# Performance work log

Measured on AMD Instinct MI355X. Metric: run time of the kernel, lower is better.

## Reference

```python
import jax, jax.numpy as jnp
import numpy as np


def build_weights(target):
    """Vectorized version of the per-(batch,frame) distance-weight loop.

    target: [B, T, W, W]. For each frame, find the mean (row, col) coordinate
    of the maximal pixels, then weight = W / (dist_to_center + 1).
    """
    W = target.shape[-1]
    m = jnp.max(target, axis=(-2, -1), keepdims=True)
    mask = (target == m).astype(target.dtype)          # [B,T,W,W]
    cnt = jnp.sum(mask, axis=(-2, -1))                 # [B,T]
    idx = jnp.arange(W, dtype=target.dtype)            # [W]
    # mean row index x and mean col index y of argmax pixels
    x = jnp.sum(jnp.sum(mask, axis=-1) * idx, axis=-1) / cnt  # [B,T]
    y = jnp.sum(jnp.sum(mask, axis=-2) * idx, axis=-1) / cnt  # [B,T]
    a = idx[None, None, :, None] - x[:, :, None, None]  # row offsets [B,T,W,1]
    b = idx[None, None, None, :] - y[:, :, None, None]  # col offsets [B,T,1,W]
    dist = jnp.sqrt(a * a + b * b)                      # [B,T,W,W]
    return W / (dist + 1.0)  # reciprocal of (sqrt(dist)+1)/W


def setup_inputs() -> dict:
    key = jax.random.key(0)
    k1, k2 = jax.random.split(key)
    B, T, W = 16, 16, 256
    inp = jax.random.uniform(k1, (B, 1, T, W, W), dtype=jnp.float32)
    tgt = jax.random.uniform(k2, (B, T, W, W), dtype=jnp.float32)
    return {"input": inp, "target": tgt}


def reference(input, target):
    p = jnp.squeeze(input, axis=1)                 # [B,T,W,W]
    w = build_weights(target)
    # torch binary_cross_entropy clamps log terms at -100
    logp = jnp.clip(jnp.log(p), -100.0)
    log1mp = jnp.clip(jnp.log1p(-p), -100.0)
    loss = -jnp.mean(w * (target * logp + (1.0 - target) * log1mp))
    return loss
```

## Files before the change

kernel.cpp:

```cpp
#include <hip/hip_runtime.h>

#define WDIM 256
#define FRAME (WDIM * WDIM)
#define NFRAMES 256
#define NTOT ((long long)NFRAMES * FRAME)

#define ACC_OFFSET 16384

__device__ inline void monoid_merge(float& m, float& cnt, float& sr, float& sc,
                                    float m2, float cnt2, float sr2, float sc2) {
    if (m2 > m) { m = m2; cnt = cnt2; sr = sr2; sc = sc2; }
    else if (m2 == m) { cnt += cnt2; sr += sr2; sc += sc2; }
}

__global__ __launch_bounds__(256)
void floss_partial(const float* __restrict__ target, float4* __restrict__ partials,
                   double* __restrict__ acc) {
    const int blk = blockIdx.x;
    const int frame = blk >> 2;
    const int quarter = blk & 3;
    const int tid = threadIdx.x;
    const int lane = tid & 63, wave = tid >> 6;

    if (blk == 0 && tid == 0) *acc = 0.0;

    const float4* __restrict__ t4 =
        (const float4*)(target + (size_t)frame * FRAME) + quarter * 4096 + tid;

    float4 v[16];
    #pragma unroll
    for (int k = 0; k < 16; ++k) v[k] = t4[k * 256];

    const float rowb = (float)(quarter * 64 + wave);
    const float colb = (float)(lane * 4);

    float m = -1.0f, cnt = 0.0f, sr = 0.0f, sc = 0.0f;
    #pragma unroll
    for (int k = 0; k < 16; ++k) {
        const float row = rowb + (float)(4 * k);
        const float vv[4] = {v[k].x, v[k].y, v[k].z, v[k].w};
        #pragma unroll
        for (int j = 0; j < 4; ++j) {
            const float val = vv[j];
            const float col = colb + (float)j;
            if (val > m)       { m = val; cnt = 1.0f; sr = row; sc = col; }
            else if (val == m) { cnt += 1.0f; sr += row; sc += col; }
        }
    }
    #pragma unroll
    for (int off = 32; off > 0; off >>= 1) {
        float m2  = __shfl_down(m, off);
        float c2  = __shfl_down(cnt, off);
        float sr2 = __shfl_down(sr, off);
        float sc2 = __shfl_down(sc, off);
        monoid_merge(m, cnt, sr, sc, m2, c2, sr2, sc2);
    }
    __shared__ float sm[4], scnt[4], ssr[4], ssc[4];
    if (lane == 0) { sm[wave] = m; scnt[wave] = cnt; ssr[wave] = sr; ssc[wave] = sc; }
    __syncthreads();
    if (tid == 0) {
        m = sm[0]; cnt = scnt[0]; sr = ssr[0]; sc = ssc[0];
        #pragma unroll
        for (int w2 = 1; w2 < 4; ++w2)
            monoid_merge(m, cnt, sr, sc, sm[w2], scnt[w2], ssr[w2], ssc[w2]);
        partials[blk] = make_float4(m, cnt, sr, sc);
    }
}

__global__ __launch_bounds__(256)
void floss_bce(const float* __restrict__ input, const float* __restrict__ target,
               const float4* __restrict__ partials, double* __restrict__ acc) {
    const int blk = blockIdx.x;
    const int frame = blk >> 3;
    const int seg = blk & 7;
    const int tid = threadIdx.x;
    const int lane = tid & 63, wave = tid >> 6;

    const float4* __restrict__ t4 =
        (const float4*)(target + (size_t)frame * FRAME) + seg * 2048 + tid;
    const float4* __restrict__ p4 =
        (const float4*)(input + (size_t)frame * FRAME) + seg * 2048 + tid;

    float4 tv[8], pv[8];
    #pragma unroll
    for (int k = 0; k < 8; ++k) { tv[k] = t4[k * 256]; pv[k] = p4[k * 256]; }

    float m, cnt, sr, sc;
    {
        const float4 p0 = partials[frame * 4 + 0];
        m = p0.x; cnt = p0.y; sr = p0.z; sc = p0.w;
        #pragma unroll
        for (int q = 1; q < 4; ++q) {
            const float4 pq = partials[frame * 4 + q];
            monoid_merge(m, cnt, sr, sc, pq.x, pq.y, pq.z, pq.w);
        }
    }
    const float rc = __builtin_amdgcn_rcpf(cnt);
    const float x = sr * rc;
    const float y = sc * rc;

    const float drb = (float)(seg * 32 + wave) - x;
    const float dcb = (float)(lane * 4) - y;
    float dc2[4];
    #pragma unroll
    for (int j = 0; j < 4; ++j) { const float d = dcb + (float)j; dc2[j] = d * d; }

    float acc0 = 0.0f, acc1 = 0.0f;
    #pragma unroll
    for (int k = 0; k < 8; ++k) {
        const float dr = drb + (float)(4 * k);
        const float dr2 = dr * dr;
        const float tvv[4] = {tv[k].x, tv[k].y, tv[k].z, tv[k].w};
        const float pvv[4] = {pv[k].x, pv[k].y, pv[k].z, pv[k].w};
        #pragma unroll
        for (int j = 0; j < 4; ++j) {
            const float dist = __builtin_amdgcn_sqrtf(dr2 + dc2[j]);
            const float w = 256.0f * __builtin_amdgcn_rcpf(dist + 1.0f);
            const float tt = tvv[j], pp = pvv[j];
            const float lp  = fmaxf(__logf(pp), -100.0f);
            const float l1p = fmaxf(__logf(1.0f - pp), -100.0f);
            if (j & 1) acc1 += w * fmaf(tt, lp - l1p, l1p);
            else       acc0 += w * fmaf(tt, lp - l1p, l1p);
        }
    }
    float local = acc0 + acc1;
    #pragma unroll
    for (int off = 32; off > 0; off >>= 1) local += __shfl_down(local, off);
    __shared__ float sacc[4];
    if (lane == 0) sacc[wave] = local;
    __syncthreads();
    if (tid == 0) {
        atomicAdd(acc, (double)(sacc[0] + sacc[1] + sacc[2] + sacc[3]));
    }
}

__global__ void floss_final(const double* __restrict__ acc, float* __restrict__ out) {
    if (threadIdx.x == 0 && blockIdx.x == 0)
        out[0] = (float)(-acc[0] / (double)NTOT);
}

extern "C" void kernel_launch(void* const* d_in, const int* in_sizes, int n_in,
                              void* d_out, int out_size, void* d_ws, size_t ws_size,
                              hipStream_t stream) {
    const float* input  = (const float*)d_in[0];
    const float* target = (const float*)d_in[1];
    float* out = (float*)d_out;
    float4* partials = (float4*)d_ws;
    double* acc = (double*)((char*)d_ws + ACC_OFFSET);

    floss_partial<<<NFRAMES * 4, 256, 0, stream>>>(target, partials, acc);
    floss_bce<<<NFRAMES * 8, 256, 0, stream>>>(input, target, partials, acc);
    floss_final<<<1, 64, 0, stream>>>(acc, out);
}
```

Measured before the change: 159.4 us.

## Fuse argmax and BCE passes per frame, caching target as bf16 in LDS

```diff
diff --git a/kernel.cpp b/kernel.cpp
--- a/kernel.cpp
+++ b/kernel.cpp
@@ -1,11 +1,13 @@
 #include <hip/hip_runtime.h>
+#include <hip/hip_bf16.h>
+#include <string.h>
 
 #define WDIM 256
 #define FRAME (WDIM * WDIM)
 #define NFRAMES 256
 #define NTOT ((long long)NFRAMES * FRAME)
+#define BLOCK 1024
 
-#define ACC_OFFSET 16384
 
 __device__ inline void monoid_merge(float& m, float& cnt, float& sr, float& sc,
                                     float m2, float cnt2, float sr2, float sc2) {
@@ -13,39 +15,41 @@
     else if (m2 == m) { cnt += cnt2; sr += sr2; sc += sc2; }
 }
 
-__global__ __launch_bounds__(256)
-void floss_partial(const float* __restrict__ target, float4* __restrict__ partials,
-                   double* __restrict__ acc) {
-    const int blk = blockIdx.x;
-    const int frame = blk >> 2;
-    const int quarter = blk & 3;
+__device__ inline unsigned int pack_bf16x2(float a, float b) {
+    __hip_bfloat162 h = __float22bfloat162_rn(make_float2(a, b));
+    unsigned int u; memcpy(&u, &h, 4); return u;
+}
+
+__global__ __launch_bounds__(BLOCK, 4)
+void floss_fused(const float* __restrict__ input, const float* __restrict__ target,
+                 double* __restrict__ blocksum) {
+    __shared__ unsigned int lds_t[FRAME / 2];
+    __shared__ float sm[16], scnt[16], ssr[16], ssc[16];
+    __shared__ float sx, sy;
+
+    const int frame = blockIdx.x;
     const int tid = threadIdx.x;
     const int lane = tid & 63, wave = tid >> 6;
 
-    if (blk == 0 && tid == 0) *acc = 0.0;
+    const float4* __restrict__ t4 = (const float4*)(target + (size_t)frame * FRAME);
+    const float4* __restrict__ p4 = (const float4*)(input  + (size_t)frame * FRAME);
 
-    const float4* __restrict__ t4 =
-        (const float4*)(target + (size_t)frame * FRAME) + quarter * 4096 + tid;
-
-    float4 v[16];
-    #pragma unroll
-    for (int k = 0; k < 16; ++k) v[k] = t4[k * 256];
-
-    const float rowb = (float)(quarter * 64 + wave);
     const float colb = (float)(lane * 4);
-
     float m = -1.0f, cnt = 0.0f, sr = 0.0f, sc = 0.0f;
     #pragma unroll
     for (int k = 0; k < 16; ++k) {
-        const float row = rowb + (float)(4 * k);
-        const float vv[4] = {v[k].x, v[k].y, v[k].z, v[k].w};
+        const int i4 = k * 1024 + tid;
+        const float4 v = t4[i4];
+        const float row = (float)(16 * k + wave);
+        const float vv[4] = {v.x, v.y, v.z, v.w};
         #pragma unroll
         for (int j = 0; j < 4; ++j) {
             const float val = vv[j];
-            const float col = colb + (float)j;
-            if (val > m)       { m = val; cnt = 1.0f; sr = row; sc = col; }
-            else if (val == m) { cnt += 1.0f; sr += row; sc += col; }
+            if (val > m)       { m = val; cnt = 1.0f; sr = row; sc = colb + (float)j; }
+            else if (val == m) { cnt += 1.0f; sr += row; sc += colb + (float)j; }
         }
+        *(uint2*)&lds_t[2 * i4] =
+            make_uint2(pack_bf16x2(v.x, v.y), pack_bf16x2(v.z, v.w));
     }
     #pragma unroll
     for (int off = 32; off > 0; off >>= 1) {
@@ -55,88 +59,79 @@
         float sc2 = __shfl_down(sc, off);
         monoid_merge(m, cnt, sr, sc, m2, c2, sr2, sc2);
     }
-    __shared__ float sm[4], scnt[4], ssr[4], ssc[4];
     if (lane == 0) { sm[wave] = m; scnt[wave] = cnt; ssr[wave] = sr; ssc[wave] = sc; }
     __syncthreads();
     if (tid == 0) {
         m = sm[0]; cnt = scnt[0]; sr = ssr[0]; sc = ssc[0];
         #pragma unroll
-        for (int w2 = 1; w2 < 4; ++w2)
+        for (int w2 = 1; w2 < 16; ++w2)
             monoid_merge(m, cnt, sr, sc, sm[w2], scnt[w2], ssr[w2], ssc[w2]);
-        partials[blk] = make_float4(m, cnt, sr, sc);
+        const float rc = __builtin_amdgcn_rcpf(cnt);
+        sx = sr * rc;
+        sy = sc * rc;
     }
-}
+    __syncthreads();
+    const float x = sx, y = sy;
 
-__global__ __launch_bounds__(256)
-void floss_bce(const float* __restrict__ input, const float* __restrict__ target,
-               const float4* __restrict__ partials, double* __restrict__ acc) {
-    const int blk = blockIdx.x;
-    const int frame = blk >> 3;
-    const int seg = blk & 7;
-    const int tid = threadIdx.x;
-    const int lane = tid & 63, wave = tid >> 6;
-
-    const float4* __restrict__ t4 =
-        (const float4*)(target + (size_t)frame * FRAME) + seg * 2048 + tid;
-    const float4* __restrict__ p4 =
-        (const float4*)(input + (size_t)frame * FRAME) + seg * 2048 + tid;
-
-    float4 tv[8], pv[8];
-    #pragma unroll
-    for (int k = 0; k < 8; ++k) { tv[k] = t4[k * 256]; pv[k] = p4[k * 256]; }
-
-    float m, cnt, sr, sc;
-    {
-        const float4 p0 = partials[frame * 4 + 0];
-        m = p0.x; cnt = p0.y; sr = p0.z; sc = p0.w;
-        #pragma unroll
-        for (int q = 1; q < 4; ++q) {
-            const float4 pq = partials[frame * 4 + q];
-            monoid_merge(m, cnt, sr, sc, pq.x, pq.y, pq.z, pq.w);
-        }
-    }
-    const float rc = __builtin_amdgcn_rcpf(cnt);
-    const float x = sr * rc;
-    const float y = sc * rc;
-
-    const float drb = (float)(seg * 32 + wave) - x;
-    const float dcb = (float)(lane * 4) - y;
+    const float drb = (float)wave - x;
     float dc2[4];
     #pragma unroll
-    for (int j = 0; j < 4; ++j) { const float d = dcb + (float)j; dc2[j] = d * d; }
+    for (int j = 0; j < 4; ++j) {
+        const float d = colb + (float)j - y;
+        dc2[j] = d * d;
+    }
 
     float acc0 = 0.0f, acc1 = 0.0f;
     #pragma unroll
-    for (int k = 0; k < 8; ++k) {
-        const float dr = drb + (float)(4 * k);
+    for (int k = 0; k < 16; ++k) {
+        const int i4 = k * 1024 + tid;
+        const float4 pvv = p4[i4];
+        const uint2 tw = *(const uint2*)&lds_t[2 * i4];
+        const float tvv[4] = {
+            __uint_as_float(tw.x << 16),
+            __uint_as_float(tw.x & 0xffff0000u),
+            __uint_as_float(tw.y << 16),
+            __uint_as_float(tw.y & 0xffff0000u)
+        };
+        const float pp[4] = {pvv.x, pvv.y, pvv.z, pvv.w};
+        const float dr = drb + (float)(16 * k);
         const float dr2 = dr * dr;
-        const float tvv[4] = {tv[k].x, tv[k].y, tv[k].z, tv[k].w};
-        const float pvv[4] = {pv[k].x, pv[k].y, pv[k].z, pv[k].w};
         #pragma unroll
         for (int j = 0; j < 4; ++j) {
             const float dist = __builtin_amdgcn_sqrtf(dr2 + dc2[j]);
             const float w = 256.0f * __builtin_amdgcn_rcpf(dist + 1.0f);
-            const float tt = tvv[j], pp = pvv[j];
-            const float lp  = fmaxf(__logf(pp), -100.0f);
-            const float l1p = fmaxf(__logf(1.0f - pp), -100.0f);
-            if (j & 1) acc1 += w * fmaf(tt, lp - l1p, l1p);
-            else       acc0 += w * fmaf(tt, lp - l1p, l1p);
+            const float p = pp[j];
+            const float lp  = fmaxf(__logf(p), -100.0f);
+            const float l1p = fmaxf(__logf(1.0f - p), -100.0f);
+            if (j & 1) acc1 += w * fmaf(tvv[j], lp - l1p, l1p);
+            else       acc0 += w * fmaf(tvv[j], lp - l1p, l1p);
         }
     }
     float local = acc0 + acc1;
     #pragma unroll
     for (int off = 32; off > 0; off >>= 1) local += __shfl_down(local, off);
-    __shared__ float sacc[4];
-    if (lane == 0) sacc[wave] = local;
+    if (lane == 0) sm[wave] = local;
     __syncthreads();
     if (tid == 0) {
-        atomicAdd(acc, (double)(sacc[0] + sacc[1] + sacc[2] + sacc[3]));
+        float s = 0.0f;
+        #pragma unroll
+        for (int w2 = 0; w2 < 16; ++w2) s += sm[w2];
+        blocksum[frame] = (double)s;
     }
 }
 
-__global__ void floss_final(const double* __restrict__ acc, float* __restrict__ out) {
-    if (threadIdx.x == 0 && blockIdx.x == 0)
-        out[0] = (float)(-acc[0] / (double)NTOT);
+__global__ __launch_bounds__(256)
+void floss_final(const double* __restrict__ blocksum, float* __restrict__ out) {
+    const int tid = threadIdx.x;
+    const int lane = tid & 63, wave = tid >> 6;
+    double v = blocksum[tid];
+    #pragma unroll
+    for (int off = 32; off > 0; off >>= 1) v += __shfl_down(v, off);
+    __shared__ double sd[4];
+    if (lane == 0) sd[wave] = v;
+    __syncthreads();
+    if (tid == 0)
+        out[0] = (float)(-(sd[0] + sd[1] + sd[2] + sd[3]) / (double)NTOT);
 }
 
 extern "C" void kernel_launch(void* const* d_in, const int* in_sizes, int n_in,
@@ -145,10 +140,8 @@
     const float* input  = (const float*)d_in[0];
     const float* target = (const float*)d_in[1];
     float* out = (float*)d_out;
-    float4* partials = (float4*)d_ws;
-    double* acc = (double*)((char*)d_ws + ACC_OFFSET);
+    double* blocksum = (double*)d_ws;
 
-    floss_partial<<<NFRAMES * 4, 256, 0, stream>>>(target, partials, acc);
-    floss_bce<<<NFRAMES * 8, 256, 0, stream>>>(input, target, partials, acc);
-    floss_final<<<1, 64, 0, stream>>>(acc, out);
+    floss_fused<<<NFRAMES, BLOCK, 0, stream>>>(input, target, blocksum);
+    floss_final<<<1, 256, 0, stream>>>(blocksum, out);
 }
```

Result: faster. 148.6 us (-6.8%).
